# Kernel tuning notes

Measured on AMD Instinct MI355X. Metric: run time of the kernel, lower is better.

Reference implementation:

```python
import jax, jax.numpy as jnp
import numpy as np

EPS = 1e-5  # torch BatchNorm default


def setup_inputs() -> dict:
    key = jax.random.key(0)
    ks = jax.random.split(key, 8)
    B, Q, S, C = 4, 256, 128, 256
    feats = [2 * C, 256, 64, 1]  # opt['num_features']
    inp = {
        "support_features": jax.random.normal(ks[0], (B, S, C), dtype=jnp.float32),
        "query_features": jax.random.normal(ks[1], (B, Q, C), dtype=jnp.float32),
    }
    for i in range(3):
        fan_in, fan_out = feats[i], feats[i + 1]
        std = np.sqrt(2.0 / (fan_in + fan_out))  # xavier_normal on conv weight
        inp[f"W{i}"] = jax.random.normal(ks[2 + i], (fan_out, fan_in), dtype=jnp.float32) * std
        inp[f"b{i}"] = jnp.zeros((fan_out,), dtype=jnp.float32)
        inp[f"g{i}"] = jnp.ones((fan_out,), dtype=jnp.float32)   # BN weight
        inp[f"bt{i}"] = jnp.zeros((fan_out,), dtype=jnp.float32)  # BN bias
    return inp


def _bn_relu(x, g, bt):
    # x: [B, N, C]; BatchNorm1d training-mode stats over batch and length dims
    mean = jnp.mean(x, axis=(0, 1))
    var = jnp.mean(jnp.square(x - mean), axis=(0, 1))  # biased var, as torch BN
    return jax.nn.relu((x - mean) * (g * jax.lax.rsqrt(var + EPS)) + bt)


def reference(support_features, query_features,
              W0, b0, g0, bt0, W1, b1, g1, bt1, W2, b2, g2, bt2):
    B, S, C = support_features.shape
    Q = query_features.shape[1]
    # pairwise concat: [B, Q, S, 2C]
    uq = jnp.broadcast_to(query_features[:, :, None, :], (B, Q, S, C))
    us = jnp.broadcast_to(support_features[:, None, :, :], (B, Q, S, C))
    x = jnp.concatenate([uq, us], axis=3).reshape(B, Q * S, 2 * C)
    # 1x1 conv == matmul over channel dim
    x = _bn_relu(jnp.einsum('bnc,oc->bno', x, W0) + b0, g0, bt0)
    x = _bn_relu(jnp.einsum('bnc,oc->bno', x, W1) + b1, g1, bt1)
    x = _bn_relu(jnp.einsum('bnc,oc->bno', x, W2) + b2, g2, bt2)
    # back to [B, C_out, Q, S]
    return jnp.transpose(x, (0, 2, 1)).reshape(B, -1, Q, S)
```

## Files before the change

### kernel.cpp

```cpp
#include <hip/hip_runtime.h>
#include <hip/hip_bf16.h>


typedef __attribute__((ext_vector_type(4))) float f32x4;
typedef __attribute__((ext_vector_type(8))) short s16x8;

#define BN_EPS 1e-5f
#define INV_N  (1.0f/131072.0f)

__device__ __forceinline__ unsigned pk_bf16(float a, float b) {
  float2 t; t.x = a; t.y = b;
  __hip_bfloat162 h = __float22bfloat162_rn(t);
  return *reinterpret_cast<unsigned*>(&h);
}
__device__ __forceinline__ void split2(float a, float b, unsigned& uh, unsigned& ul) {
  uh = pk_bf16(a, b);
  float ha = __uint_as_float(uh << 16);
  float hb = __uint_as_float(uh & 0xFFFF0000u);
  ul = pk_bf16(a - ha, b - hb);
}

union frag_u { s16x8 v; unsigned u[4]; };

struct Args {
  const float *Sf, *Qf, *W0, *b0, *g0, *bt0, *W1, *b1, *g1, *bt1, *W2, *b2, *g2, *bt2;
  float *Aq, *As, *y2, *ws0s, *ws1f, *ws2f, *out;
  ushort *W1h, *W1l, *y1f;
};

__global__ __launch_bounds__(256) void k_g0(Args a)
{
  int bi = blockIdx.x, t = threadIdx.x;
  if (bi == 96) {
    for (int k = 0; k < 32; k++) {
      int idx = t * 64 + k * 2;
      unsigned uh, ul;
      split2(a.W1[idx], a.W1[idx + 1], uh, ul);
      a.W1h[idx] = (ushort)(uh & 0xFFFFu); a.W1h[idx + 1] = (ushort)(uh >> 16);
      a.W1l[idx] = (ushort)(ul & 0xFFFFu); a.W1l[idx + 1] = (ushort)(ul >> 16);
    }
    for (int i = t; i < 2048; i += 256) a.ws1f[i] = 0.0f;
    if (t < 32) a.ws2f[t] = 0.0f;
    return;
  }
  int w = t >> 6, l = t & 63, l15 = l & 15, quad = l >> 4;
  bool isQ = (bi < 64);
  const float* X; float* Out; int m0, koff;
  if (isQ) { m0 = bi * 16; X = a.Qf; Out = a.Aq; koff = 0; }
  else     { m0 = (bi - 64) * 16; X = a.Sf; Out = a.As; koff = 256; }
  int n0 = w * 64;

  f32x4 acc[4] = {};
#pragma unroll
  for (int ko = 0; ko < 256; ko += 32) {
    const float* row = X + (m0 + l15) * 256 + ko + quad * 8;
    f32x4 v0 = *(const f32x4*)(row);
    f32x4 v1 = *(const f32x4*)(row + 4);
    frag_u ah, al;
#pragma unroll
    for (int j = 0; j < 2; j++) {
      split2(v0[2 * j], v0[2 * j + 1], ah.u[j], al.u[j]);
      split2(v1[2 * j], v1[2 * j + 1], ah.u[2 + j], al.u[2 + j]);
    }
#pragma unroll
    for (int nt = 0; nt < 4; nt++) {
      const float* wrow = a.W0 + (n0 + nt * 16 + l15) * 512 + koff + ko + quad * 8;
      f32x4 w0v = *(const f32x4*)(wrow);
      f32x4 w1v = *(const f32x4*)(wrow + 4);
      frag_u bh, bl;
      split2(w0v[0], w0v[1], bh.u[0], bl.u[0]);
      split2(w0v[2], w0v[3], bh.u[1], bl.u[1]);
      split2(w1v[0], w1v[1], bh.u[2], bl.u[2]);
      split2(w1v[2], w1v[3], bh.u[3], bl.u[3]);
      acc[nt] = __builtin_amdgcn_mfma_f32_16x16x32_bf16(ah.v, bh.v, acc[nt], 0, 0, 0);
      acc[nt] = __builtin_amdgcn_mfma_f32_16x16x32_bf16(al.v, bh.v, acc[nt], 0, 0, 0);
      acc[nt] = __builtin_amdgcn_mfma_f32_16x16x32_bf16(ah.v, bl.v, acc[nt], 0, 0, 0);
    }
  }
#pragma unroll
  for (int nt = 0; nt < 4; nt++) {
    int o = n0 + nt * 16 + l15;
    float bias = isQ ? 0.0f : a.b0[o];
    float cs = 0, cs2 = 0;
#pragma unroll
    for (int r = 0; r < 4; r++) {
      float y = acc[nt][r] + bias;
      Out[(m0 + quad * 4 + r) * 256 + o] = y;
      cs += y; cs2 += y * y;
    }
    cs  += __shfl_xor(cs, 16);  cs  += __shfl_xor(cs, 32);
    cs2 += __shfl_xor(cs2, 16); cs2 += __shfl_xor(cs2, 32);
    if (quad == 0) {
      a.ws0s[bi * 512 + o] = cs;
      a.ws0s[bi * 512 + 256 + o] = cs2;
    }
  }
}

__device__ __forceinline__ void bn0_finalize(const Args& a, int t, float* sh_a0c0)
{
  int o = t;
  float sumY = 0, cross = 0, SQ2 = 0, SS2 = 0;
#pragma unroll
  for (int b = 0; b < 4; b++) {
    float sq1 = 0, sq2 = 0, ss1 = 0, ss2 = 0;
#pragma unroll
    for (int c = 0; c < 16; c++) {
      sq1 += a.ws0s[(b * 16 + c) * 512 + o];
      sq2 += a.ws0s[(b * 16 + c) * 512 + 256 + o];
    }
#pragma unroll
    for (int c = 0; c < 8; c++) {
      ss1 += a.ws0s[(64 + b * 8 + c) * 512 + o];
      ss2 += a.ws0s[(64 + b * 8 + c) * 512 + 256 + o];
    }
    SQ2 += sq2; SS2 += ss2;
    sumY += 128.0f * sq1 + 256.0f * ss1;
    cross += sq1 * ss1;
  }
  float mean = sumY * INV_N;
  float var = (128.0f * SQ2 + 256.0f * SS2 + 2.0f * cross) * INV_N - mean * mean;
  float aa = a.g0[o] * rsqrtf(var + BN_EPS);
  sh_a0c0[o] = aa;
  sh_a0c0[256 + o] = a.bt0[o] - mean * aa;
}

__global__ __launch_bounds__(256) void k_m1(Args a)
{
  int bi = blockIdx.x, t = threadIdx.x;
  int w = t >> 6, l = t & 63, l15 = l & 15, quad = l >> 4;
  __shared__ ushort w1hf[2048 * 8];
  __shared__ ushort w1lf[2048 * 8];
  __shared__ float sh_a0c0[512];
  __shared__ float red[2][4][4][16];

#pragma unroll
  for (int i = 0; i < 8; i++) {
    int fr = i * 256 + t;
    int kk = fr >> 8, r = fr & 255, nt = r >> 6, ln = r & 63;
    int src = (nt * 16 + (ln & 15)) * 256 + kk * 32 + (ln >> 4) * 8;
    *(s16x8*)(w1hf + fr * 8) = *(const s16x8*)(a.W1h + src);
    *(s16x8*)(w1lf + fr * 8) = *(const s16x8*)(a.W1l + src);
  }
  bn0_finalize(a, t, sh_a0c0);
  __syncthreads();

  int b_ = bi >> 7, rem = bi & 127, qt = rem >> 3, st = rem & 7;
  const float* asrow = a.As + ((b_ << 7) + st * 16 + l15) * 256;
  const float* aqrow[4];
#pragma unroll
  for (int mt = 0; mt < 4; mt++)
    aqrow[mt] = a.Aq + ((b_ << 8) + qt * 16 + w * 4 + mt) * 256;

  f32x4 acc[4][4] = {};
#pragma unroll
  for (int kk = 0; kk < 8; kk++) {
    int obase = kk * 32 + quad * 8;
    f32x4 a0v0 = *(const f32x4*)(sh_a0c0 + obase);
    f32x4 a0v1 = *(const f32x4*)(sh_a0c0 + obase + 4);
    f32x4 c0v0 = *(const f32x4*)(sh_a0c0 + 256 + obase);
    f32x4 c0v1 = *(const f32x4*)(sh_a0c0 + 256 + obase + 4);
    f32x4 as0 = *(const f32x4*)(asrow + obase);
    f32x4 as1 = *(const f32x4*)(asrow + obase + 4);

    s16x8 zh[4];
#pragma unroll
    for (int mt = 0; mt < 4; mt++) {
      f32x4 aq0 = *(const f32x4*)(aqrow[mt] + obase);
      f32x4 aq1 = *(const f32x4*)(aqrow[mt] + obase + 4);
      f32x4 z0 = (aq0 + as0) * a0v0 + c0v0;
      f32x4 z1 = (aq1 + as1) * a0v1 + c0v1;
      frag_u zz;
      zz.u[0] = pk_bf16(fmaxf(z0[0], 0.0f), fmaxf(z0[1], 0.0f));
      zz.u[1] = pk_bf16(fmaxf(z0[2], 0.0f), fmaxf(z0[3], 0.0f));
      zz.u[2] = pk_bf16(fmaxf(z1[0], 0.0f), fmaxf(z1[1], 0.0f));
      zz.u[3] = pk_bf16(fmaxf(z1[2], 0.0f), fmaxf(z1[3], 0.0f));
      zh[mt] = zz.v;
    }
#pragma unroll
    for (int nt = 0; nt < 4; nt++) {
      s16x8 bh = *(const s16x8*)(w1hf + ((kk * 4 + nt) * 64 + l) * 8);
      s16x8 bl = *(const s16x8*)(w1lf + ((kk * 4 + nt) * 64 + l) * 8);
#pragma unroll
      for (int mt = 0; mt < 4; mt++) {
        acc[mt][nt] = __builtin_amdgcn_mfma_f32_16x16x32_bf16(zh[mt], bh, acc[mt][nt], 0, 0, 0);
        acc[mt][nt] = __builtin_amdgcn_mfma_f32_16x16x32_bf16(zh[mt], bl, acc[mt][nt], 0, 0, 0);
      }
    }
  }

  float biasv[4];
#pragma unroll
  for (int nt = 0; nt < 4; nt++) biasv[nt] = a.b1[nt * 16 + l15];
  float s[4] = {0, 0, 0, 0}, s2[4] = {0, 0, 0, 0};
#pragma unroll
  for (int mt = 0; mt < 4; mt++) {
#pragma unroll
    for (int nt = 0; nt < 4; nt++) {
      float y0 = acc[mt][nt][0] + biasv[nt];
      float y1 = acc[mt][nt][1] + biasv[nt];
      float y2v = acc[mt][nt][2] + biasv[nt];
      float y3 = acc[mt][nt][3] + biasv[nt];
      unsigned u01 = pk_bf16(y0, y1), u23 = pk_bf16(y2v, y3);
      uint2 pk; pk.x = u01; pk.y = u23;
      int slot = (bi * 4 + w) * 16 + mt * 4 + nt;
      *(uint2*)(a.y1f + (size_t)(slot * 64 + l) * 4) = pk;
      float f0 = __uint_as_float(u01 << 16), f1 = __uint_as_float(u01 & 0xFFFF0000u);
      float f2 = __uint_as_float(u23 << 16), f3 = __uint_as_float(u23 & 0xFFFF0000u);
      s[nt]  += f0 + f1 + f2 + f3;
      s2[nt] += f0 * f0 + f1 * f1 + f2 * f2 + f3 * f3;
    }
  }
#pragma unroll
  for (int nt = 0; nt < 4; nt++) {
    float v = s[nt], v2 = s2[nt];
    v  += __shfl_xor(v, 16);  v  += __shfl_xor(v, 32);
    v2 += __shfl_xor(v2, 16); v2 += __shfl_xor(v2, 32);
    if (quad == 0) { red[0][w][nt][l15] = v; red[1][w][nt][l15] = v2; }
  }
  __syncthreads();
  if (t < 128) {
    int which = t >> 6, j = t & 63, nt = j >> 4, jl = j & 15;
    float v = red[which][0][nt][jl] + red[which][1][nt][jl] +
              red[which][2][nt][jl] + red[which][3][nt][jl];
    atomicAdd(&a.ws1f[(bi & 15) * 128 + t], v);
  }
}

__global__ __launch_bounds__(256) void k_p2(Args a)
{
  int p = blockIdx.x, t = threadIdx.x;
  int w = t >> 6, l = t & 63, l15 = l & 15, quad = l >> 4;
  __shared__ float sh_tot[128];
  __shared__ float sh_a1c1[128];
  __shared__ float rs[16], rs2[16];

  if (t < 128) {
    float accv = 0;
#pragma unroll
    for (int c = 0; c < 16; c++) accv += a.ws1f[c * 128 + t];
    sh_tot[t] = accv;
  }
  __syncthreads();
  if (t < 64) {
    float mean = sh_tot[t] * INV_N;
    float var = sh_tot[64 + t] * INV_N - mean * mean;
    float aa = a.g1[t] * rsqrtf(var + BN_EPS);
    sh_a1c1[t] = aa;
    sh_a1c1[64 + t] = a.bt1[t] - mean * aa;
  }
  __syncthreads();

  float a1v[4], c1v[4], w2v[4];
#pragma unroll
  for (int nt = 0; nt < 4; nt++) {
    int j = nt * 16 + l15;
    a1v[nt] = sh_a1c1[j]; c1v[nt] = sh_a1c1[64 + j]; w2v[nt] = a.W2[j];
  }
  float b2v = a.b2[0];
  float ls = 0, ls2 = 0;

#pragma unroll
  for (int task = 0; task < 2; task++) {
    int gw = (p * 4 + w) * 2 + task;
    int bi = gw >> 2, w1 = gw & 3;
    int b = bi >> 7, rem = bi & 127, qt = rem >> 3, st = rem & 7;
#pragma unroll
    for (int mt = 0; mt < 4; mt++) {
      float part[4] = {0, 0, 0, 0};
#pragma unroll
      for (int nt = 0; nt < 4; nt++) {
        int slot = (bi * 4 + w1) * 16 + mt * 4 + nt;
        uint2 v = *(const uint2*)(a.y1f + (size_t)(slot * 64 + l) * 4);
        float f0 = __uint_as_float(v.x << 16), f1 = __uint_as_float(v.x & 0xFFFF0000u);
        float f2 = __uint_as_float(v.y << 16), f3 = __uint_as_float(v.y & 0xFFFF0000u);
        part[0] += fmaxf(a1v[nt] * f0 + c1v[nt], 0.0f) * w2v[nt];
        part[1] += fmaxf(a1v[nt] * f1 + c1v[nt], 0.0f) * w2v[nt];
        part[2] += fmaxf(a1v[nt] * f2 + c1v[nt], 0.0f) * w2v[nt];
        part[3] += fmaxf(a1v[nt] * f3 + c1v[nt], 0.0f) * w2v[nt];
      }
#pragma unroll
      for (int r = 0; r < 4; r++) {
        float pv = part[r];
        pv += __shfl_xor(pv, 1); pv += __shfl_xor(pv, 2);
        pv += __shfl_xor(pv, 4); pv += __shfl_xor(pv, 8);
        part[r] = pv + b2v;
      }
      if (l15 == 0) {
        int q = qt * 16 + w1 * 4 + mt;
        int P = ((b * 256 + q) * 128) + st * 16 + quad * 4;
        f32x4 o;
#pragma unroll
        for (int r = 0; r < 4; r++) { o[r] = part[r]; ls += part[r]; ls2 += part[r] * part[r]; }
        *(f32x4*)(a.y2 + P) = o;
      }
    }
  }
  if (l15 == 0) { rs[t >> 4] = ls; rs2[t >> 4] = ls2; }
  __syncthreads();
  if (t == 0) {
    float sv = 0, sv2 = 0;
#pragma unroll
    for (int i = 0; i < 16; i++) { sv += rs[i]; sv2 += rs2[i]; }
    atomicAdd(&a.ws2f[(p & 15) * 2], sv);
    atomicAdd(&a.ws2f[(p & 15) * 2 + 1], sv2);
  }
}

__global__ __launch_bounds__(256) void k_out(Args a)
{
  int t = threadIdx.x;
  float s = 0, s2 = 0;
#pragma unroll
  for (int c = 0; c < 16; c++) { s += a.ws2f[c * 2]; s2 += a.ws2f[c * 2 + 1]; }
  float mean = s * INV_N;
  float var = s2 * INV_N - mean * mean;
  float aa = a.g2[0] * rsqrtf(var + BN_EPS);
  float cc = a.bt2[0] - mean * aa;
  int i = (blockIdx.x * 256 + t) * 4;
  f32x4 v = *(const f32x4*)(a.y2 + i);
  f32x4 o;
#pragma unroll
  for (int r = 0; r < 4; r++) o[r] = fmaxf(aa * v[r] + cc, 0.0f);
  *(f32x4*)(a.out + i) = o;
}

extern "C" void kernel_launch(void* const* d_in, const int* in_sizes, int n_in,
                              void* d_out, int out_size, void* d_ws, size_t ws_size,
                              hipStream_t stream)
{
  float* ws = (float*)d_ws;
  Args a;
  a.Sf  = (const float*)d_in[0];
  a.Qf  = (const float*)d_in[1];
  a.W0  = (const float*)d_in[2];
  a.b0  = (const float*)d_in[3];
  a.g0  = (const float*)d_in[4];
  a.bt0 = (const float*)d_in[5];
  a.W1  = (const float*)d_in[6];
  a.b1  = (const float*)d_in[7];
  a.g1  = (const float*)d_in[8];
  a.bt1 = (const float*)d_in[9];
  a.W2  = (const float*)d_in[10];
  a.b2  = (const float*)d_in[11];
  a.g2  = (const float*)d_in[12];
  a.bt2 = (const float*)d_in[13];

  a.Aq   = ws;
  a.As   = ws + 262144;
  a.y2   = ws + 393216;
  a.ws0s = ws + 524288;
  a.ws1f = ws + 573440;
  a.ws2f = ws + 575488;
  a.W1h  = (ushort*)(ws + 575552);
  a.W1l  = (ushort*)(ws + 583744);
  a.y1f  = (ushort*)(ws + 591936);
  a.out  = (float*)d_out;

  k_g0 <<<97, 256, 0, stream>>>(a);
  k_m1 <<<512, 256, 0, stream>>>(a);
  k_p2 <<<256, 256, 0, stream>>>(a);
  k_out<<<128, 256, 0, stream>>>(a);
}
```

Before: 137.6 us.

## Drop split-bf16 W1 correction and convert W1 in-block; split first GEMM blocks

The second-layer GEMM now uses a single bf16 copy of W1, converted from fp32 directly while staging into shared memory. The separate hi/lo split, its workspace buffers and the extra correction MFMA per tile are gone. This halves the MFMA work and the weight LDS traffic in k_m1. The first GEMM kernel is also relaunched as 385 single-wave blocks instead of 97 four-wave blocks, which spreads work across more CUs. The cost is lower precision in layer 1, whose weights are no longer split into hi and lo parts.

```diff
diff --git a/kernel.cpp b/kernel.cpp
--- a/kernel.cpp
+++ b/kernel.cpp
@@ -25,30 +25,24 @@
 struct Args {
   const float *Sf, *Qf, *W0, *b0, *g0, *bt0, *W1, *b1, *g1, *bt1, *W2, *b2, *g2, *bt2;
   float *Aq, *As, *y2, *ws0s, *ws1f, *ws2f, *out;
-  ushort *W1h, *W1l, *y1f;
+  ushort *y1f;
 };
 
-__global__ __launch_bounds__(256) void k_g0(Args a)
+__global__ __launch_bounds__(64) void k_g0(Args a)
 {
   int bi = blockIdx.x, t = threadIdx.x;
-  if (bi == 96) {
-    for (int k = 0; k < 32; k++) {
-      int idx = t * 64 + k * 2;
-      unsigned uh, ul;
-      split2(a.W1[idx], a.W1[idx + 1], uh, ul);
-      a.W1h[idx] = (ushort)(uh & 0xFFFFu); a.W1h[idx + 1] = (ushort)(uh >> 16);
-      a.W1l[idx] = (ushort)(ul & 0xFFFFu); a.W1l[idx + 1] = (ushort)(ul >> 16);
-    }
-    for (int i = t; i < 2048; i += 256) a.ws1f[i] = 0.0f;
+  if (bi == 384) {
+    for (int i = t; i < 2048; i += 64) a.ws1f[i] = 0.0f;
     if (t < 32) a.ws2f[t] = 0.0f;
     return;
   }
-  int w = t >> 6, l = t & 63, l15 = l & 15, quad = l >> 4;
-  bool isQ = (bi < 64);
+  int l15 = t & 15, quad = t >> 4;
+  int chunk = bi >> 2, ntile = bi & 3;
+  bool isQ = (chunk < 64);
   const float* X; float* Out; int m0, koff;
-  if (isQ) { m0 = bi * 16; X = a.Qf; Out = a.Aq; koff = 0; }
-  else     { m0 = (bi - 64) * 16; X = a.Sf; Out = a.As; koff = 256; }
-  int n0 = w * 64;
+  if (isQ) { m0 = chunk * 16; X = a.Qf; Out = a.Aq; koff = 0; }
+  else     { m0 = (chunk - 64) * 16; X = a.Sf; Out = a.As; koff = 256; }
+  int n0 = ntile * 64;
 
   f32x4 acc[4] = {};
 #pragma unroll
@@ -91,8 +85,8 @@
     cs  += __shfl_xor(cs, 16);  cs  += __shfl_xor(cs, 32);
     cs2 += __shfl_xor(cs2, 16); cs2 += __shfl_xor(cs2, 32);
     if (quad == 0) {
-      a.ws0s[bi * 512 + o] = cs;
-      a.ws0s[bi * 512 + 256 + o] = cs2;
+      a.ws0s[chunk * 512 + o] = cs;
+      a.ws0s[chunk * 512 + 256 + o] = cs2;
     }
   }
 }
@@ -129,8 +123,7 @@
 {
   int bi = blockIdx.x, t = threadIdx.x;
   int w = t >> 6, l = t & 63, l15 = l & 15, quad = l >> 4;
-  __shared__ ushort w1hf[2048 * 8];
-  __shared__ ushort w1lf[2048 * 8];
+  __shared__ ushort w1f[2048 * 8];
   __shared__ float sh_a0c0[512];
   __shared__ float red[2][4][4][16];
 
@@ -138,9 +131,13 @@
   for (int i = 0; i < 8; i++) {
     int fr = i * 256 + t;
     int kk = fr >> 8, r = fr & 255, nt = r >> 6, ln = r & 63;
-    int src = (nt * 16 + (ln & 15)) * 256 + kk * 32 + (ln >> 4) * 8;
-    *(s16x8*)(w1hf + fr * 8) = *(const s16x8*)(a.W1h + src);
-    *(s16x8*)(w1lf + fr * 8) = *(const s16x8*)(a.W1l + src);
+    const float* src = a.W1 + (nt * 16 + (ln & 15)) * 256 + kk * 32 + (ln >> 4) * 8;
+    f32x4 v0 = *(const f32x4*)(src);
+    f32x4 v1 = *(const f32x4*)(src + 4);
+    frag_u z;
+    z.u[0] = pk_bf16(v0[0], v0[1]); z.u[1] = pk_bf16(v0[2], v0[3]);
+    z.u[2] = pk_bf16(v1[0], v1[1]); z.u[3] = pk_bf16(v1[2], v1[3]);
+    *(s16x8*)(w1f + fr * 8) = z.v;
   }
   bn0_finalize(a, t, sh_a0c0);
   __syncthreads();
@@ -179,13 +176,10 @@
     }
 #pragma unroll
     for (int nt = 0; nt < 4; nt++) {
-      s16x8 bh = *(const s16x8*)(w1hf + ((kk * 4 + nt) * 64 + l) * 8);
-      s16x8 bl = *(const s16x8*)(w1lf + ((kk * 4 + nt) * 64 + l) * 8);
-#pragma unroll
-      for (int mt = 0; mt < 4; mt++) {
-        acc[mt][nt] = __builtin_amdgcn_mfma_f32_16x16x32_bf16(zh[mt], bh, acc[mt][nt], 0, 0, 0);
-        acc[mt][nt] = __builtin_amdgcn_mfma_f32_16x16x32_bf16(zh[mt], bl, acc[mt][nt], 0, 0, 0);
-      }
+      s16x8 bw = *(const s16x8*)(w1f + ((kk * 4 + nt) * 64 + l) * 8);
+#pragma unroll
+      for (int mt = 0; mt < 4; mt++)
+        acc[mt][nt] = __builtin_amdgcn_mfma_f32_16x16x32_bf16(zh[mt], bw, acc[mt][nt], 0, 0, 0);
     }
   }
 
@@ -352,12 +346,10 @@
   a.ws0s = ws + 524288;
   a.ws1f = ws + 573440;
   a.ws2f = ws + 575488;
-  a.W1h  = (ushort*)(ws + 575552);
-  a.W1l  = (ushort*)(ws + 583744);
-  a.y1f  = (ushort*)(ws + 591936);
+  a.y1f  = (ushort*)(ws + 575552);
   a.out  = (float*)d_out;
 
-  k_g0 <<<97, 256, 0, stream>>>(a);
+  k_g0 <<<385, 64, 0, stream>>>(a);
   k_m1 <<<512, 256, 0, stream>>>(a);
   k_p2 <<<256, 256, 0, stream>>>(a);
   k_out<<<128, 256, 0, stream>>>(a);
```

Result: faster. 132.0 us (-4.1%).
